# Performance work log

Hardware: AMD Instinct MI355X
Metric: run time of the kernel (lower is better)

## Reference

```python
import jax, jax.numpy as jnp
import numpy as np

NEG = -999999.0

def setup_inputs() -> dict:
    key = jax.random.key(0)
    ks = jax.random.split(key, 8)
    B, N, H, D = 8, 2048, 1, 256  # in_dim = H*D = 256
    in_dim = H * D
    feat_in = jax.random.normal(ks[0], (B, N, in_dim), dtype=jnp.float32)
    adj = jax.random.randint(ks[1], (B, N, N), 0, 2, dtype=jnp.int32)
    # parameters (xavier-ish scales)
    W  = jax.random.normal(ks[2], (H, in_dim, D), dtype=jnp.float32) * (2.0 / (in_dim + D)) ** 0.5
    b  = jnp.zeros((D,), dtype=jnp.float32)
    Ws = jax.random.normal(ks[3], (1, 2 * D), dtype=jnp.float32) * (2.0 / (2 * D + 1)) ** 0.5  # strengh.weight
    bs = jnp.zeros((1,), dtype=jnp.float32)                                                     # strengh.bias
    Hw = jax.random.normal(ks[4], (in_dim, in_dim), dtype=jnp.float32) * (1.0 / in_dim) ** 0.5  # H.weight
    Hb = jnp.zeros((in_dim,), dtype=jnp.float32)                                                # H.bias
    return {"feat_in": feat_in, "adj": adj, "W": W, "b": b, "Ws": Ws, "bs": bs, "Hw": Hw, "Hb": Hb}

def reference(feat_in, adj, W, b, Ws, bs, Hw, Hb):
    B, N, in_dim = feat_in.shape
    H, _, D = W.shape
    h = jnp.einsum('bni,hid->bhnd', feat_in, W)                    # [B,H,N,D]
    # strengh(cat(h_src, h_dst)) decomposed: H_src[b,i,j]=h[b,i], H_dst[b,i,j]=h[b,j]
    ws_src, ws_dst = Ws[0, :D], Ws[0, D:]
    a_src = jnp.einsum('bhnd,d->bhn', h, ws_src)                   # per row i
    a_dst = jnp.einsum('bhnd,d->bhn', h, ws_dst)                   # per col j
    attn = jax.nn.sigmoid(a_src[:, :, :, None] + a_dst[:, :, None, :] + bs[0])  # [B,H,N,N]
    strict_low = jnp.tril(jnp.ones((N, N), dtype=feat_in.dtype), -1)
    attn = attn * strict_low                                        # zero outside strict lower triangle
    I_A = jnp.eye(N, dtype=feat_in.dtype) - attn                    # [B,H,N,N]
    I_A_raw = I_A
    # allowed positions: lower triangle (incl diag) AND adj==1
    low = jnp.tril(jnp.ones((N, N), dtype=jnp.bool_), 0)
    allowed = low[None, None] & (adj[:, None] == 1)                 # [B,H,N,N]
    scores = jnp.where(allowed, I_A, NEG)
    P = jax.nn.softmax(scores, axis=-1)
    feat_out = jnp.einsum('bhij,bhjd->bhid', P, h) + b              # [B,H,N,D]
    feat_out = feat_out.transpose(0, 2, 1, 3).reshape(B, N, H * D)
    feat_out = jax.nn.elu(feat_out)
    gate = jax.nn.sigmoid(feat_in @ Hw.T + Hb)
    out = gate * feat_out + (1.0 - gate) * feat_in                  # dropout = identity (eval)
    return out, I_A_raw
```

## Files before the change

### kernel.cpp

```cpp
#include <hip/hip_runtime.h>
#include <math.h>

constexpr int Bc = 8, Nc = 2048, Dc = 256;
constexpr int BN = Bc * Nc;

typedef __attribute__((ext_vector_type(8))) short short8;
typedef __attribute__((ext_vector_type(4))) float f32x4;

__device__ __forceinline__ float sigmoidf_(float x) { return 1.0f / (1.0f + expf(-x)); }

__device__ __forceinline__ unsigned short f2bf(float f) {
    unsigned int u = __float_as_uint(f);
    u = (u + 0x7FFFu + ((u >> 16) & 1u)) >> 16;
    return (unsigned short)u;
}

__device__ __forceinline__ short8 ld_frag(const unsigned short* base) {
    ushort4 lo = *(const ushort4*)(base);
    ushort4 hi = *(const ushort4*)(base + 16);
    short8 a;
    a[0] = (short)lo.x; a[1] = (short)lo.y; a[2] = (short)lo.z; a[3] = (short)lo.w;
    a[4] = (short)hi.x; a[5] = (short)hi.y; a[6] = (short)hi.z; a[7] = (short)hi.w;
    return a;
}

__device__ __forceinline__ f32x4 fz4() { f32x4 z = {0.f, 0.f, 0.f, 0.f}; return z; }

__global__ __launch_bounds__(256) void cast_kernel(const float* __restrict__ f,
                                                   unsigned short* __restrict__ o) {
    int i = (blockIdx.x * 256 + threadIdx.x) * 4;
    float4 v = *(const float4*)(f + i);
    ushort4 u = {f2bf(v.x), f2bf(v.y), f2bf(v.z), f2bf(v.w)};
    *(ushort4*)(o + i) = u;
}

__global__ __launch_bounds__(256) void pack_bt_kernel(const float* __restrict__ W,
                                                      const float* __restrict__ Hw,
                                                      unsigned short* __restrict__ BmT) {
    int idx = blockIdx.x * 256 + threadIdx.x;
    int o = idx >> 8, k = idx & 255;
    float v = (o < 256) ? W[k * 256 + o] : Hw[(o - 256) * 256 + k];
    BmT[idx] = f2bf(v);
}

__global__ __launch_bounds__(256) void gemm_mfma(const unsigned short* __restrict__ featb,
                                                 const unsigned short* __restrict__ BmT,
                                                 const float* __restrict__ Hb,
                                                 float* __restrict__ h,
                                                 float* __restrict__ gate) {
    const int tid = threadIdx.x, lane = tid & 63, w = tid >> 6;
    const int g16 = lane >> 4, li = lane & 15;
    const int m0 = blockIdx.x * 64, nw = blockIdx.y * 128 + w * 32;
    f32x4 acc[4][2];
#pragma unroll
    for (int rf = 0; rf < 4; ++rf)
#pragma unroll
        for (int cf = 0; cf < 2; ++cf) acc[rf][cf] = fz4();
    for (int k0 = 0; k0 < 256; k0 += 32) {
        short8 Af[4];
#pragma unroll
        for (int rf = 0; rf < 4; ++rf)
            Af[rf] = ld_frag(featb + (size_t)(m0 + rf * 16 + li) * 256 + k0 + g16 * 4);
#pragma unroll
        for (int cf = 0; cf < 2; ++cf) {
            short8 Bf = ld_frag(BmT + (size_t)(nw + cf * 16 + li) * 256 + k0 + g16 * 4);
#pragma unroll
            for (int rf = 0; rf < 4; ++rf)
                acc[rf][cf] = __builtin_amdgcn_mfma_f32_16x16x32_bf16(Af[rf], Bf, acc[rf][cf], 0, 0, 0);
        }
    }
#pragma unroll
    for (int rf = 0; rf < 4; ++rf)
#pragma unroll
        for (int cf = 0; cf < 2; ++cf) {
            const int n = nw + cf * 16 + li;
#pragma unroll
            for (int reg = 0; reg < 4; ++reg) {
                const int m = m0 + rf * 16 + g16 * 4 + reg;
                float v = acc[rf][cf][reg];
                if (n < 256) h[(size_t)m * 256 + n] = v;
                else gate[(size_t)m * 256 + (n - 256)] = sigmoidf_(v + Hb[n - 256]);
            }
        }
}

__global__ __launch_bounds__(256) void tr64_kernel(const float* __restrict__ h,
                                                   unsigned short* __restrict__ hT) {
    __shared__ float tile[64][65];
    const int j0 = blockIdx.x * 64, d0 = blockIdx.y * 64, b = blockIdx.z;
    const int tid = threadIdx.x;
#pragma unroll
    for (int p = 0; p < 16; ++p) {
        int idx = tid + p * 256;
        int jl = idx >> 6, dl = idx & 63;
        tile[jl][dl] = h[((size_t)b * Nc + j0 + jl) * 256 + d0 + dl];
    }
    __syncthreads();
#pragma unroll
    for (int p = 0; p < 16; ++p) {
        int idx = tid + p * 256;
        int dl = idx >> 6, jl = idx & 63;
        hT[((size_t)b * 256 + d0 + dl) * Nc + j0 + jl] = f2bf(tile[jl][dl]);
    }
}

__global__ __launch_bounds__(256) void asrc_kernel(const float* __restrict__ h,
                                                   const float* __restrict__ Ws,
                                                   float* __restrict__ a_src,
                                                   float* __restrict__ a_dst) {
    const int row = blockIdx.x * 4 + (threadIdx.x >> 6);
    const int lane = threadIdx.x & 63;
    float4 h4 = ((const float4*)(h + (size_t)row * 256))[lane];
    float4 ws = ((const float4*)Ws)[lane];
    float4 wd = ((const float4*)(Ws + 256))[lane];
    float s1 = h4.x * ws.x + h4.y * ws.y + h4.z * ws.z + h4.w * ws.w;
    float s2 = h4.x * wd.x + h4.y * wd.y + h4.z * wd.z + h4.w * wd.w;
#pragma unroll
    for (int m = 32; m >= 1; m >>= 1) {
        s1 += __shfl_xor(s1, m, 64);
        s2 += __shfl_xor(s2, m, 64);
    }
    if (lane == 0) { a_src[row] = s1; a_dst[row] = s2; }
}

__global__ __launch_bounds__(256) void mean_kernel(const float* __restrict__ h,
                                                   float* __restrict__ mean_h) {
    const int blk = blockIdx.x;
    const int b = blk >> 5, part = blk & 31;
    const int d = threadIdx.x;
    float sum = 0.f;
    const float* base = h + ((size_t)b * Nc + part * 64) * 256 + d;
#pragma unroll 4
    for (int r = 0; r < 64; ++r) sum += base[(size_t)r * 256];
    atomicAdd(&mean_h[b * 256 + d], sum);
}

constexpr int CHUNK = 8;
__global__ __launch_bounds__(256) void score_mfma(
    const int* __restrict__ adj, const unsigned short* __restrict__ hT,
    const float* __restrict__ a_src, const float* __restrict__ a_dst,
    const float* __restrict__ bs_p, float* __restrict__ out2,
    float* __restrict__ accO, float* __restrict__ sArr) {
    __shared__ unsigned short pt[32][40];
    __shared__ float sh_as[32];

    const int bid = blockIdx.x;
    const int b = bid & 7;
    int t = bid >> 3;
    int g = 0;
    while (g < 7 && 4 * (g + 1) * (g + 2) <= t) ++g;
    const int r_ = t - 4 * g * (g + 1);
    const int ib = g * 8 + r_ / (g + 1);
    const int c = r_ % (g + 1);
    const int i0 = ib * 32;
    const int t0 = c * CHUNK;
    const int t1 = min(ib + 1, t0 + CHUNK);

    const int tid = threadIdx.x;
    const int lane = tid & 63;
    const int w = tid >> 6;
    const int g16 = lane >> 4, li = lane & 15;
    const int jj_ = tid & 31;
    const int r0 = tid >> 5;
    const float bsv = bs_p[0];

    if (tid < 32) sh_as[tid] = a_src[b * Nc + i0 + tid];
    __syncthreads();

    f32x4 acc[2][4];
#pragma unroll
    for (int rf = 0; rf < 2; ++rf)
#pragma unroll
        for (int cf = 0; cf < 4; ++cf) acc[rf][cf] = fz4();
    f32x4 sacc0 = fz4(), sacc1 = fz4();
    short8 ones;
#pragma unroll
    for (int e = 0; e < 8; ++e) ones[e] = (short)0x3F80;

    const unsigned short* hTb = hT + (size_t)b * 256 * Nc;

    for (int tt = t0; tt < t1; ++tt) {
        const int j0 = tt * 32;
        if (tt > t0) __syncthreads();
        {
            const int j = j0 + jj_;
            const float adstj = a_dst[b * Nc + j];
#pragma unroll
            for (int q = 0; q < 4; ++q) {
                const int r = r0 + 8 * q;
                const int i = i0 + r;
                const int av = adj[((size_t)b * Nc + i) * Nc + j];
                float IA, p;
                if (j > i) { IA = 0.f; p = 0.f; }
                else {
                    IA = (j == i) ? 1.f : -sigmoidf_(sh_as[r] + adstj + bsv);
                    out2[((size_t)b * Nc + i) * Nc + j] = IA;
                    p = (av == 1) ? expf(IA - 1.f) : 0.f;
                }
                pt[r][jj_] = f2bf(p);
            }
        }
        __syncthreads();
        {
            short8 A0 = ld_frag(&pt[li][g16 * 4]);
            short8 A1 = ld_frag(&pt[16 + li][g16 * 4]);
            if (w == 0) {
                sacc0 = __builtin_amdgcn_mfma_f32_16x16x32_bf16(A0, ones, sacc0, 0, 0, 0);
                sacc1 = __builtin_amdgcn_mfma_f32_16x16x32_bf16(A1, ones, sacc1, 0, 0, 0);
            }
#pragma unroll
            for (int cf = 0; cf < 4; ++cf) {
                const unsigned short* bp =
                    hTb + (size_t)(w * 64 + cf * 16 + li) * Nc + j0 + g16 * 4;
                short8 Bf = ld_frag(bp);
                acc[0][cf] = __builtin_amdgcn_mfma_f32_16x16x32_bf16(A0, Bf, acc[0][cf], 0, 0, 0);
                acc[1][cf] = __builtin_amdgcn_mfma_f32_16x16x32_bf16(A1, Bf, acc[1][cf], 0, 0, 0);
            }
        }
    }
#pragma unroll
    for (int rf = 0; rf < 2; ++rf)
#pragma unroll
        for (int cf = 0; cf < 4; ++cf) {
            const int row = i0 + rf * 16 + g16 * 4;
            float* dst = accO + ((size_t)b * Nc + row) * 256 + w * 64 + cf * 16 + li;
#pragma unroll
            for (int reg = 0; reg < 4; ++reg)
                atomicAdd(dst + (size_t)reg * 256, acc[rf][cf][reg]);
        }
    if (w == 0 && li == 0) {
#pragma unroll
        for (int reg = 0; reg < 4; ++reg) {
            atomicAdd(&sArr[b * Nc + i0 + g16 * 4 + reg], sacc0[reg]);
            atomicAdd(&sArr[b * Nc + i0 + 16 + g16 * 4 + reg], sacc1[reg]);
        }
    }
}

__global__ __launch_bounds__(256) void epilogue_kernel(
    const float* __restrict__ gate, const float* __restrict__ feat,
    const float* __restrict__ bvec, const float* __restrict__ mean_h,
    const float* __restrict__ sArr, float* __restrict__ out1) {
    const int row = blockIdx.x * 4 + (threadIdx.x >> 6);
    const int lane = threadIdx.x & 63;
    const int b = row >> 11;
    const size_t g = (size_t)row * 256;
    const float s = sArr[row];
    float4 v;
    if (s == 0.f) {
        float4 mh = ((const float4*)(mean_h + b * 256))[lane];
        const float inv = 1.0f / Nc;
        v.x = mh.x * inv; v.y = mh.y * inv; v.z = mh.z * inv; v.w = mh.w * inv;
    } else {
        float4 a = ((const float4*)(out1 + g))[lane];
        const float inv = 1.0f / s;
        v.x = a.x * inv; v.y = a.y * inv; v.z = a.z * inv; v.w = a.w * inv;
    }
    const float4 b4 = ((const float4*)bvec)[lane];
    v.x += b4.x; v.y += b4.y; v.z += b4.z; v.w += b4.w;
    v.x = v.x > 0.f ? v.x : expf(v.x) - 1.f;
    v.y = v.y > 0.f ? v.y : expf(v.y) - 1.f;
    v.z = v.z > 0.f ? v.z : expf(v.z) - 1.f;
    v.w = v.w > 0.f ? v.w : expf(v.w) - 1.f;
    const float4 g4 = ((const float4*)(gate + g))[lane];
    const float4 f4 = ((const float4*)(feat + g))[lane];
    float4 o;
    o.x = g4.x * v.x + (1.f - g4.x) * f4.x;
    o.y = g4.y * v.y + (1.f - g4.y) * f4.y;
    o.z = g4.z * v.z + (1.f - g4.z) * f4.z;
    o.w = g4.w * v.w + (1.f - g4.w) * f4.w;
    ((float4*)(out1 + g))[lane] = o;
}

extern "C" void kernel_launch(void* const* d_in, const int* in_sizes, int n_in,
                              void* d_out, int out_size, void* d_ws, size_t ws_size,
                              hipStream_t stream) {
    const float* feat = (const float*)d_in[0];
    const int* adj = (const int*)d_in[1];
    const float* W = (const float*)d_in[2];
    const float* bvec = (const float*)d_in[3];
    const float* Ws = (const float*)d_in[4];
    const float* bs = (const float*)d_in[5];
    const float* Hw = (const float*)d_in[6];
    const float* Hb = (const float*)d_in[7];

    float* ws = (float*)d_ws;
    unsigned short* featb = (unsigned short*)ws;
    unsigned short* hT = featb;
    unsigned short* BmT = featb + 4194304;
    float* h = ws + 2097152 + 65536;
    float* gate = h + 4194304;
    float* a_src = gate + 4194304;
    float* a_dst = a_src + 16384;
    float* mean_h = a_dst + 16384;
    float* sArr = mean_h + 2048;

    float* out1 = (float*)d_out;
    float* out2 = out1 + (size_t)BN * 256;

    hipLaunchKernelGGL(cast_kernel, dim3(4096), dim3(256), 0, stream, feat, featb);
    hipLaunchKernelGGL(pack_bt_kernel, dim3(512), dim3(256), 0, stream, W, Hw, BmT);
    hipLaunchKernelGGL(gemm_mfma, dim3(256, 4), dim3(256), 0, stream, featb, BmT, Hb, h, gate);
    hipLaunchKernelGGL(tr64_kernel, dim3(32, 4, 8), dim3(256), 0, stream, h, hT);
    hipLaunchKernelGGL(asrc_kernel, dim3(4096), dim3(256), 0, stream, h, Ws, a_src, a_dst);
    hipMemsetAsync(mean_h, 0, 2048 * sizeof(float), stream);
    hipLaunchKernelGGL(mean_kernel, dim3(256), dim3(256), 0, stream, h, mean_h);
    hipMemsetAsync(sArr, 0, (size_t)BN * sizeof(float), stream);
    hipMemsetAsync(out1, 0, (size_t)BN * 256 * sizeof(float), stream);
    hipMemsetAsync(out2, 0, (size_t)BN * (size_t)Nc * sizeof(float), stream);
    hipLaunchKernelGGL(score_mfma, dim3(2304), dim3(256), 0, stream,
                       adj, hT, a_src, a_dst, bs, out2, out1, sArr);
    hipLaunchKernelGGL(epilogue_kernel, dim3(4096), dim3(256), 0, stream,
                       gate, feat, bvec, mean_h, sArr, out1);
}
```

Before: 454.8 us.

## Tile GEMM via LDS, fuse row-dot and mean into transpose, replace full out2 memset

The projection GEMM now stages 128x128 tiles in LDS, giving more reuse per block. The separate a_src/a_dst and mean kernels are folded into the transpose kernel using the shared tile and atomics. The full memset of the N×N attention output is replaced by a kernel that zeroes only the strict upper region, since the score kernel now writes every lower-triangle entry. The score kernel processes two 32-column tiles per barrier, prefetches adj and a_dst registers ahead, and uses fast exp/rcp. The risks are more atomics, looser numerics from the fast intrinsics, and more register pressure.

```diff
diff --git a/kernel.cpp b/kernel.cpp
--- a/kernel.cpp
+++ b/kernel.cpp
@@ -13,6 +13,9 @@
     unsigned int u = __float_as_uint(f);
     u = (u + 0x7FFFu + ((u >> 16) & 1u)) >> 16;
     return (unsigned short)u;
+}
+__device__ __forceinline__ float bf2f(unsigned short s) {
+    return __uint_as_float(((unsigned int)s) << 16);
 }
 
 __device__ __forceinline__ short8 ld_frag(const unsigned short* base) {
@@ -23,8 +26,13 @@
     a[4] = (short)hi.x; a[5] = (short)hi.y; a[6] = (short)hi.z; a[7] = (short)hi.w;
     return a;
 }
-
 __device__ __forceinline__ f32x4 fz4() { f32x4 z = {0.f, 0.f, 0.f, 0.f}; return z; }
+
+__device__ __forceinline__ void lds_barrier() {
+    asm volatile("s_waitcnt lgkmcnt(0)" ::: "memory");
+    __builtin_amdgcn_s_barrier();
+    __builtin_amdgcn_sched_barrier(0);
+}
 
 __global__ __launch_bounds__(256) void cast_kernel(const float* __restrict__ f,
                                                    unsigned short* __restrict__ o) {
@@ -43,40 +51,57 @@
     BmT[idx] = f2bf(v);
 }
 
-__global__ __launch_bounds__(256) void gemm_mfma(const unsigned short* __restrict__ featb,
-                                                 const unsigned short* __restrict__ BmT,
-                                                 const float* __restrict__ Hb,
-                                                 float* __restrict__ h,
-                                                 float* __restrict__ gate) {
+__global__ __launch_bounds__(256) void gemm_lds(const unsigned short* __restrict__ featb,
+                                                const unsigned short* __restrict__ BmT,
+                                                const float* __restrict__ Hb,
+                                                float* __restrict__ h,
+                                                float* __restrict__ gate) {
+    __shared__ unsigned short As[128][72];
+    __shared__ unsigned short Bs[128][72];
     const int tid = threadIdx.x, lane = tid & 63, w = tid >> 6;
     const int g16 = lane >> 4, li = lane & 15;
-    const int m0 = blockIdx.x * 64, nw = blockIdx.y * 128 + w * 32;
-    f32x4 acc[4][2];
+    const int wr = w >> 1, wc = w & 1;
+    const int m0 = blockIdx.x * 128, n0 = blockIdx.y * 128;
+    const int srow = tid >> 1, sseg = (tid & 1) * 32;
+    f32x4 acc[4][4];
 #pragma unroll
     for (int rf = 0; rf < 4; ++rf)
 #pragma unroll
-        for (int cf = 0; cf < 2; ++cf) acc[rf][cf] = fz4();
-    for (int k0 = 0; k0 < 256; k0 += 32) {
-        short8 Af[4];
-#pragma unroll
-        for (int rf = 0; rf < 4; ++rf)
-            Af[rf] = ld_frag(featb + (size_t)(m0 + rf * 16 + li) * 256 + k0 + g16 * 4);
-#pragma unroll
-        for (int cf = 0; cf < 2; ++cf) {
-            short8 Bf = ld_frag(BmT + (size_t)(nw + cf * 16 + li) * 256 + k0 + g16 * 4);
+        for (int cf = 0; cf < 4; ++cf) acc[rf][cf] = fz4();
+    for (int k0 = 0; k0 < 256; k0 += 64) {
+        if (k0) __syncthreads();
+#pragma unroll
+        for (int q = 0; q < 4; ++q) {
+            int4 va = *(const int4*)(featb + (size_t)(m0 + srow) * 256 + k0 + sseg + q * 8);
+            *(int4*)&As[srow][sseg + q * 8] = va;
+            int4 vb = *(const int4*)(BmT + (size_t)(n0 + srow) * 256 + k0 + sseg + q * 8);
+            *(int4*)&Bs[srow][sseg + q * 8] = vb;
+        }
+        __syncthreads();
+#pragma unroll
+        for (int ks = 0; ks < 2; ++ks) {
+            short8 Af[4], Bf[4];
 #pragma unroll
             for (int rf = 0; rf < 4; ++rf)
-                acc[rf][cf] = __builtin_amdgcn_mfma_f32_16x16x32_bf16(Af[rf], Bf, acc[rf][cf], 0, 0, 0);
+                Af[rf] = ld_frag(&As[wr * 64 + rf * 16 + li][ks * 32 + g16 * 4]);
+#pragma unroll
+            for (int cf = 0; cf < 4; ++cf)
+                Bf[cf] = ld_frag(&Bs[wc * 64 + cf * 16 + li][ks * 32 + g16 * 4]);
+#pragma unroll
+            for (int rf = 0; rf < 4; ++rf)
+#pragma unroll
+                for (int cf = 0; cf < 4; ++cf)
+                    acc[rf][cf] = __builtin_amdgcn_mfma_f32_16x16x32_bf16(Af[rf], Bf[cf], acc[rf][cf], 0, 0, 0);
         }
     }
 #pragma unroll
     for (int rf = 0; rf < 4; ++rf)
 #pragma unroll
-        for (int cf = 0; cf < 2; ++cf) {
-            const int n = nw + cf * 16 + li;
+        for (int cf = 0; cf < 4; ++cf) {
+            const int n = n0 + wc * 64 + cf * 16 + li;
 #pragma unroll
             for (int reg = 0; reg < 4; ++reg) {
-                const int m = m0 + rf * 16 + g16 * 4 + reg;
+                const int m = m0 + wr * 64 + rf * 16 + g16 * 4 + reg;
                 float v = acc[rf][cf][reg];
                 if (n < 256) h[(size_t)m * 256 + n] = v;
                 else gate[(size_t)m * 256 + (n - 256)] = sigmoidf_(v + Hb[n - 256]);
@@ -84,8 +109,12 @@
         }
 }
 
-__global__ __launch_bounds__(256) void tr64_kernel(const float* __restrict__ h,
-                                                   unsigned short* __restrict__ hT) {
+__global__ __launch_bounds__(256) void tr64f_kernel(const float* __restrict__ h,
+                                                    const float* __restrict__ Ws,
+                                                    unsigned short* __restrict__ hT,
+                                                    float* __restrict__ a_src,
+                                                    float* __restrict__ a_dst,
+                                                    float* __restrict__ mean_h) {
     __shared__ float tile[64][65];
     const int j0 = blockIdx.x * 64, d0 = blockIdx.y * 64, b = blockIdx.z;
     const int tid = threadIdx.x;
@@ -102,46 +131,51 @@
         int dl = idx >> 6, jl = idx & 63;
         hT[((size_t)b * 256 + d0 + dl) * Nc + j0 + jl] = f2bf(tile[jl][dl]);
     }
-}
-
-__global__ __launch_bounds__(256) void asrc_kernel(const float* __restrict__ h,
-                                                   const float* __restrict__ Ws,
-                                                   float* __restrict__ a_src,
-                                                   float* __restrict__ a_dst) {
-    const int row = blockIdx.x * 4 + (threadIdx.x >> 6);
-    const int lane = threadIdx.x & 63;
-    float4 h4 = ((const float4*)(h + (size_t)row * 256))[lane];
-    float4 ws = ((const float4*)Ws)[lane];
-    float4 wd = ((const float4*)(Ws + 256))[lane];
-    float s1 = h4.x * ws.x + h4.y * ws.y + h4.z * ws.z + h4.w * ws.w;
-    float s2 = h4.x * wd.x + h4.y * wd.y + h4.z * wd.z + h4.w * wd.w;
-#pragma unroll
-    for (int m = 32; m >= 1; m >>= 1) {
-        s1 += __shfl_xor(s1, m, 64);
-        s2 += __shfl_xor(s2, m, 64);
-    }
-    if (lane == 0) { a_src[row] = s1; a_dst[row] = s2; }
-}
-
-__global__ __launch_bounds__(256) void mean_kernel(const float* __restrict__ h,
-                                                   float* __restrict__ mean_h) {
-    const int blk = blockIdx.x;
-    const int b = blk >> 5, part = blk & 31;
-    const int d = threadIdx.x;
-    float sum = 0.f;
-    const float* base = h + ((size_t)b * Nc + part * 64) * 256 + d;
-#pragma unroll 4
-    for (int r = 0; r < 64; ++r) sum += base[(size_t)r * 256];
-    atomicAdd(&mean_h[b * 256 + d], sum);
+    {
+        const int jl = tid >> 2, q = tid & 3;
+        float s1 = 0.f, s2 = 0.f;
+#pragma unroll
+        for (int e = 0; e < 16; ++e) {
+            const float hv = tile[jl][q * 16 + e];
+            s1 = fmaf(hv, Ws[d0 + q * 16 + e], s1);
+            s2 = fmaf(hv, Ws[256 + d0 + q * 16 + e], s2);
+        }
+        s1 += __shfl_xor(s1, 1); s1 += __shfl_xor(s1, 2);
+        s2 += __shfl_xor(s2, 1); s2 += __shfl_xor(s2, 2);
+        if (q == 0) {
+            atomicAdd(&a_src[b * Nc + j0 + jl], s1);
+            atomicAdd(&a_dst[b * Nc + j0 + jl], s2);
+        }
+    }
+    {
+        const int dl = tid & 63, part = tid >> 6;
+        float sm = 0.f;
+#pragma unroll
+        for (int e = 0; e < 16; ++e) sm += tile[part * 16 + e][dl];
+        atomicAdd(&mean_h[b * 256 + d0 + dl], sm);
+    }
+}
+
+__global__ __launch_bounds__(256) void fill_kernel(float* __restrict__ out2) {
+    const int b = blockIdx.x & 7, ib = blockIdx.x >> 3;
+    const int j0 = (ib + 1) * 32;
+    if (j0 >= Nc) return;
+    const int i0 = ib * 32;
+    const int w4 = (Nc - j0) >> 2;
+    const float4 z = make_float4(0.f, 0.f, 0.f, 0.f);
+    for (int r = 0; r < 32; ++r) {
+        float4* row = (float4*)(out2 + ((size_t)b * Nc + i0 + r) * Nc + j0);
+        for (int jc = threadIdx.x; jc < w4; jc += 256) row[jc] = z;
+    }
 }
 
 constexpr int CHUNK = 8;
-__global__ __launch_bounds__(256) void score_mfma(
+__global__ __launch_bounds__(256) void score64(
     const int* __restrict__ adj, const unsigned short* __restrict__ hT,
     const float* __restrict__ a_src, const float* __restrict__ a_dst,
     const float* __restrict__ bs_p, float* __restrict__ out2,
     float* __restrict__ accO, float* __restrict__ sArr) {
-    __shared__ unsigned short pt[32][40];
+    __shared__ unsigned short pt[32][72];
     __shared__ float sh_as[32];
 
     const int bid = blockIdx.x;
@@ -156,16 +190,20 @@
     const int t0 = c * CHUNK;
     const int t1 = min(ib + 1, t0 + CHUNK);
 
-    const int tid = threadIdx.x;
-    const int lane = tid & 63;
-    const int w = tid >> 6;
+    const int tid = threadIdx.x, lane = tid & 63, w = tid >> 6;
     const int g16 = lane >> 4, li = lane & 15;
-    const int jj_ = tid & 31;
-    const int r0 = tid >> 5;
+    const int jj = tid & 31, r0 = tid >> 5;
     const float bsv = bs_p[0];
 
     if (tid < 32) sh_as[tid] = a_src[b * Nc + i0 + tid];
     __syncthreads();
+    float asv[4];
+#pragma unroll
+    for (int q = 0; q < 4; ++q) asv[q] = sh_as[r0 + 8 * q];
+
+    const int* adjb = adj + (size_t)b * Nc * Nc;
+    const float* adb = a_dst + b * Nc;
+    const unsigned short* hTb = hT + (size_t)b * 256 * Nc;
 
     f32x4 acc[2][4];
 #pragma unroll
@@ -177,53 +215,80 @@
 #pragma unroll
     for (int e = 0; e < 8; ++e) ones[e] = (short)0x3F80;
 
-    const unsigned short* hTb = hT + (size_t)b * 256 * Nc;
-
-    for (int tt = t0; tt < t1; ++tt) {
-        const int j0 = tt * 32;
-        if (tt > t0) __syncthreads();
-        {
-            const int j = j0 + jj_;
-            const float adstj = a_dst[b * Nc + j];
-#pragma unroll
-            for (int q = 0; q < 4; ++q) {
-                const int r = r0 + 8 * q;
-                const int i = i0 + r;
-                const int av = adj[((size_t)b * Nc + i) * Nc + j];
-                float IA, p;
-                if (j > i) { IA = 0.f; p = 0.f; }
-                else {
-                    IA = (j == i) ? 1.f : -sigmoidf_(sh_as[r] + adstj + bsv);
-                    out2[((size_t)b * Nc + i) * Nc + j] = IA;
-                    p = (av == 1) ? expf(IA - 1.f) : 0.f;
+    int pre_aj[2][4];
+    float pre_ad[2];
+#define PREF(TT, NS)                                                                   \
+    {                                                                                  \
+        _Pragma("unroll") for (int s = 0; s < 2; ++s) if (s < (NS)) {                  \
+            pre_ad[s] = adb[((TT) + s) * 32 + jj];                                     \
+            _Pragma("unroll") for (int q = 0; q < 4; ++q)                              \
+                pre_aj[s][q] = adjb[(size_t)(i0 + r0 + 8 * q) * Nc + ((TT) + s) * 32 + jj]; \
+        }                                                                              \
+    }
+
+    PREF(t0, min(2, t1 - t0));
+    for (int tt = t0; tt < t1; tt += 2) {
+        const int ns = min(2, t1 - tt);
+        int aj_[2][4];
+        float ad_[2];
+#pragma unroll
+        for (int s = 0; s < 2; ++s) {
+            ad_[s] = pre_ad[s];
+#pragma unroll
+            for (int q = 0; q < 4; ++q) aj_[s][q] = pre_aj[s][q];
+        }
+        if (tt + 2 < t1) PREF(tt + 2, min(2, t1 - tt - 2));
+        short8 Bf[2][4];
+#pragma unroll
+        for (int s = 0; s < 2; ++s)
+            if (s < ns) {
+#pragma unroll
+                for (int cf = 0; cf < 4; ++cf)
+                    Bf[s][cf] = ld_frag(hTb + (size_t)(w * 64 + cf * 16 + li) * Nc + (tt + s) * 32 + g16 * 4);
+            }
+#pragma unroll
+        for (int s = 0; s < 2; ++s)
+            if (s < ns) {
+                const int jt = tt + s;
+                const int j = jt * 32 + jj;
+                const bool dia = (jt == ib);
+#pragma unroll
+                for (int q = 0; q < 4; ++q) {
+                    const int r = r0 + 8 * q;
+                    const int irow = i0 + r;
+                    const float IA = -__builtin_amdgcn_rcpf(1.f + __expf(-(asv[q] + ad_[s] + bsv)));
+                    float o2v, p;
+                    if (dia && j > irow) { o2v = 0.f; p = 0.f; }
+                    else if (dia && j == irow) { o2v = 1.f; p = (aj_[s][q] == 1) ? 1.f : 0.f; }
+                    else { o2v = IA; p = (aj_[s][q] == 1) ? __expf(IA - 1.f) : 0.f; }
+                    out2[((size_t)b * Nc + irow) * Nc + j] = o2v;
+                    pt[r][s * 32 + jj] = f2bf(p);
                 }
-                pt[r][jj_] = f2bf(p);
             }
-        }
-        __syncthreads();
-        {
-            short8 A0 = ld_frag(&pt[li][g16 * 4]);
-            short8 A1 = ld_frag(&pt[16 + li][g16 * 4]);
-            if (w == 0) {
-                sacc0 = __builtin_amdgcn_mfma_f32_16x16x32_bf16(A0, ones, sacc0, 0, 0, 0);
-                sacc1 = __builtin_amdgcn_mfma_f32_16x16x32_bf16(A1, ones, sacc1, 0, 0, 0);
+        lds_barrier();
+#pragma unroll
+        for (int s = 0; s < 2; ++s)
+            if (s < ns) {
+                short8 A0 = ld_frag(&pt[li][s * 32 + g16 * 4]);
+                short8 A1 = ld_frag(&pt[16 + li][s * 32 + g16 * 4]);
+                if (w == 0) {
+                    sacc0 = __builtin_amdgcn_mfma_f32_16x16x32_bf16(A0, ones, sacc0, 0, 0, 0);
+                    sacc1 = __builtin_amdgcn_mfma_f32_16x16x32_bf16(A1, ones, sacc1, 0, 0, 0);
+                }
+#pragma unroll
+                for (int cf = 0; cf < 4; ++cf) {
+                    acc[0][cf] = __builtin_amdgcn_mfma_f32_16x16x32_bf16(A0, Bf[s][cf], acc[0][cf], 0, 0, 0);
+                    acc[1][cf] = __builtin_amdgcn_mfma_f32_16x16x32_bf16(A1, Bf[s][cf], acc[1][cf], 0, 0, 0);
+                }
             }
-#pragma unroll
-            for (int cf = 0; cf < 4; ++cf) {
-                const unsigned short* bp =
-                    hTb + (size_t)(w * 64 + cf * 16 + li) * Nc + j0 + g16 * 4;
-                short8 Bf = ld_frag(bp);
-                acc[0][cf] = __builtin_amdgcn_mfma_f32_16x16x32_bf16(A0, Bf, acc[0][cf], 0, 0, 0);
-                acc[1][cf] = __builtin_amdgcn_mfma_f32_16x16x32_bf16(A1, Bf, acc[1][cf], 0, 0, 0);
-            }
-        }
-    }
+        lds_barrier();
+    }
+#undef PREF
 #pragma unroll
     for (int rf = 0; rf < 2; ++rf)
 #pragma unroll
         for (int cf = 0; cf < 4; ++cf) {
-            const int row = i0 + rf * 16 + g16 * 4;
-            float* dst = accO + ((size_t)b * Nc + row) * 256 + w * 64 + cf * 16 + li;
+            float* dst = accO + ((size_t)b * Nc + i0 + rf * 16 + g16 * 4) * 256 + w * 64 + cf * 16 + li;
 #pragma unroll
             for (int reg = 0; reg < 4; ++reg)
                 atomicAdd(dst + (size_t)reg * 256, acc[rf][cf][reg]);
@@ -258,10 +323,10 @@
     }
     const float4 b4 = ((const float4*)bvec)[lane];
     v.x += b4.x; v.y += b4.y; v.z += b4.z; v.w += b4.w;
-    v.x = v.x > 0.f ? v.x : expf(v.x) - 1.f;
-    v.y = v.y > 0.f ? v.y : expf(v.y) - 1.f;
-    v.z = v.z > 0.f ? v.z : expf(v.z) - 1.f;
-    v.w = v.w > 0.f ? v.w : expf(v.w) - 1.f;
+    v.x = v.x > 0.f ? v.x : __expf(v.x) - 1.f;
+    v.y = v.y > 0.f ? v.y : __expf(v.y) - 1.f;
+    v.z = v.z > 0.f ? v.z : __expf(v.z) - 1.f;
+    v.w = v.w > 0.f ? v.w : __expf(v.w) - 1.f;
     const float4 g4 = ((const float4*)(gate + g))[lane];
     const float4 f4 = ((const float4*)(feat + g))[lane];
     float4 o;
@@ -300,15 +365,13 @@
 
     hipLaunchKernelGGL(cast_kernel, dim3(4096), dim3(256), 0, stream, feat, featb);
     hipLaunchKernelGGL(pack_bt_kernel, dim3(512), dim3(256), 0, stream, W, Hw, BmT);
-    hipLaunchKernelGGL(gemm_mfma, dim3(256, 4), dim3(256), 0, stream, featb, BmT, Hb, h, gate);
-    hipLaunchKernelGGL(tr64_kernel, dim3(32, 4, 8), dim3(256), 0, stream, h, hT);
-    hipLaunchKernelGGL(asrc_kernel, dim3(4096), dim3(256), 0, stream, h, Ws, a_src, a_dst);
-    hipMemsetAsync(mean_h, 0, 2048 * sizeof(float), stream);
-    hipLaunchKernelGGL(mean_kernel, dim3(256), dim3(256), 0, stream, h, mean_h);
-    hipMemsetAsync(sArr, 0, (size_t)BN * sizeof(float), stream);
+    hipLaunchKernelGGL(gemm_lds, dim3(128, 4), dim3(256), 0, stream, featb, BmT, Hb, h, gate);
+    hipMemsetAsync(a_src, 0, (16384 + 16384 + 2048 + 16384) * sizeof(float), stream);
+    hipLaunchKernelGGL(tr64f_kernel, dim3(32, 4, 8), dim3(256), 0, stream,
+                       h, Ws, hT, a_src, a_dst, mean_h);
     hipMemsetAsync(out1, 0, (size_t)BN * 256 * sizeof(float), stream);
-    hipMemsetAsync(out2, 0, (size_t)BN * (size_t)Nc * sizeof(float), stream);
-    hipLaunchKernelGGL(score_mfma, dim3(2304), dim3(256), 0, stream,
+    hipLaunchKernelGGL(fill_kernel, dim3(512), dim3(256), 0, stream, out2);
+    hipLaunchKernelGGL(score64, dim3(2304), dim3(256), 0, stream,
                        adj, hT, a_src, a_dst, bs, out2, out1, sArr);
     hipLaunchKernelGGL(epilogue_kernel, dim3(4096), dim3(256), 0, stream,
                        gate, feat, bvec, mean_h, sArr, out1);
```

Result: faster. 389.3 us (-14.4%).
